# Performance work log

Hardware: AMD Instinct MI355X
Metric: run time of the kernel (lower is better)

## Reference

```python
import jax, jax.numpy as jnp
import numpy as np

N_NODES = 100000
N_EDGES = 3200000
IN_DIM = 768
HIDDEN = 128
CLASS_NUM = 2
N_GRAPHS = 512


def setup_inputs() -> dict:
    key = jax.random.key(0)
    ks = jax.random.split(key, 10)
    x = jax.random.normal(ks[0], (N_NODES, IN_DIM), dtype=jnp.float32)
    edge_index = jax.random.randint(ks[1], (2, N_EDGES), 0, N_NODES, dtype=jnp.int64)
    ptr = jnp.sort(jax.random.randint(ks[2], (N_GRAPHS + 1,), 0, N_NODES, dtype=jnp.int64))
    def glorot(k, shape):
        lim = jnp.sqrt(6.0 / (shape[0] + shape[1]))
        return jax.random.uniform(k, shape, jnp.float32, -lim, lim)
    W1 = glorot(ks[3], (IN_DIM, HIDDEN))
    b1 = jnp.zeros((HIDDEN,), jnp.float32)
    W2 = glorot(ks[4], (HIDDEN, HIDDEN))
    b2 = jnp.zeros((HIDDEN,), jnp.float32)
    Wc = glorot(ks[5], (HIDDEN, CLASS_NUM))
    bc = jnp.zeros((CLASS_NUM,), jnp.float32)
    return {"x": x, "edge_index": edge_index, "ptr": ptr,
            "W1": W1, "b1": b1, "W2": W2, "b2": b2, "Wc": Wc, "bc": bc}


def _gcn_conv(x, W, b, src, dst, norm, n_nodes):
    # PyG GCNConv: linear first, then normalized scatter-add aggregation, then bias
    h = x @ W                                  # [N, out]
    msg = h[src] * norm[:, None]               # gather + scale, [E+N, out]
    out = jax.ops.segment_sum(msg, dst, num_segments=n_nodes)
    return out + b


def reference(x, edge_index, ptr, W1, b1, W2, b2, Wc, bc):
    n = x.shape[0]
    loop = jnp.arange(n, dtype=edge_index.dtype)
    src = jnp.concatenate([edge_index[0], loop])  # add self-loops
    dst = jnp.concatenate([edge_index[1], loop])
    deg = jax.ops.segment_sum(jnp.ones_like(dst, dtype=x.dtype), dst, num_segments=n)
    dinv = jnp.where(deg > 0, jax.lax.rsqrt(deg), 0.0)
    norm = dinv[src] * dinv[dst]               # symmetric normalization
    h = jax.nn.relu(_gcn_conv(x, W1, b1, src, dst, norm, n))
    h = jax.nn.relu(_gcn_conv(h, W2, b2, src, dst, norm, n))
    out = _gcn_conv(h, Wc, bc, src, dst, norm, n)
    return out[ptr[:-1]]                       # first_pool: first node of each graph
```

## Files before the change

kernel.cpp:

```cpp
#include <hip/hip_runtime.h>

typedef short bf16x8 __attribute__((ext_vector_type(8)));
typedef float f32x4 __attribute__((ext_vector_type(4)));
typedef _Float16 f16x4 __attribute__((ext_vector_type(4)));

__device__ __forceinline__ unsigned short f2bf_rn(float x) {
    unsigned int u = __float_as_uint(x);
    unsigned int r = u + 0x7FFF + ((u >> 16) & 1);
    return (unsigned short)(r >> 16);
}
__device__ __forceinline__ float bf2f(unsigned short h) {
    return __uint_as_float(((unsigned int)h) << 16);
}


__global__ __launch_bounds__(256) void bucket_hist(const int* __restrict__ ei,
                                                   int* __restrict__ bcnt, int E, int NB) {
    __shared__ int h[1024];
    for (int i = threadIdx.x; i < NB; i += 256) h[i] = 0;
    __syncthreads();
    for (int e = blockIdx.x * blockDim.x + threadIdx.x; e < E; e += gridDim.x * blockDim.x) {
        atomicAdd(&h[ei[E + e] >> 7], 1);
    }
    __syncthreads();
    for (int i = threadIdx.x; i < NB; i += 256) {
        int v = h[i];
        if (v) atomicAdd(&bcnt[i], v);
    }
}

__global__ __launch_bounds__(1024) void bucket_scan(const int* __restrict__ bcnt,
                                                    int* __restrict__ bbase,
                                                    int* __restrict__ bcur,
                                                    int* __restrict__ offs,
                                                    int NB, int NN, int E) {
    __shared__ int s[1024];
    int t = threadIdx.x;
    int v = (t < NB) ? bcnt[t] : 0;
    s[t] = v;
    __syncthreads();
    for (int off = 1; off < 1024; off <<= 1) {
        int u = (t >= off) ? s[t - off] : 0;
        __syncthreads();
        s[t] += u;
        __syncthreads();
    }
    if (t < NB) {
        int base = s[t] - v;
        bbase[t] = base;
        bcur[t] = base;
    }
    if (t == 0) {
        bbase[NB] = E;
        offs[NN] = E;
    }
}

__global__ __launch_bounds__(256) void bucket_scatter(const int* __restrict__ ei,
                                                      int* __restrict__ bcur,
                                                      unsigned int* __restrict__ epk,
                                                      int E, int NB) {
    __shared__ int hist[1024];
    __shared__ int cur[1024];
    int tid = threadIdx.x;
    int chunk = (E + gridDim.x - 1) / gridDim.x;
    int beg = blockIdx.x * chunk;
    int end = beg + chunk; if (end > E) end = E;
    for (int i = tid; i < NB; i += 256) hist[i] = 0;
    __syncthreads();
    for (int e = beg + tid; e < end; e += 256) {
        atomicAdd(&hist[ei[E + e] >> 7], 1);
    }
    __syncthreads();
    for (int i = tid; i < NB; i += 256) {
        int c = hist[i];
        cur[i] = c ? atomicAdd(&bcur[i], c) : 0;
    }
    __syncthreads();
    for (int e = beg + tid; e < end; e += 256) {
        int s = ei[e];
        int d = ei[E + e];
        int p = atomicAdd(&cur[d >> 7], 1);
        epk[p] = ((unsigned)(d & 127) << 17) | (unsigned)s;
    }
}

__global__ __launch_bounds__(256) void bucket_build(const unsigned int* __restrict__ epk,
                                                    const int* __restrict__ bbase,
                                                    int* __restrict__ offs,
                                                    float* __restrict__ dinv,
                                                    int* __restrict__ srt,
                                                    int NN) {
    __shared__ int lcnt[128];
    __shared__ int sc[128];
    __shared__ int lcur[128];
    int b = blockIdx.x;
    int tid = threadIdx.x;
    int base = bbase[b], endp = bbase[b + 1];
    int ne = endp - base;
    int v0 = b << 7;
    int nv = NN - v0; if (nv > 128) nv = 128;

    if (tid < 128) lcnt[tid] = 0;
    __syncthreads();
    for (int i = tid; i < ne; i += 256) {
        int d = (int)(epk[base + i] >> 17);
        atomicAdd(&lcnt[d], 1);
    }
    __syncthreads();
    if (tid < 128) sc[tid] = lcnt[tid];
    __syncthreads();
    for (int off = 1; off < 128; off <<= 1) {
        int u = (tid < 128 && tid >= off) ? sc[tid - off] : 0;
        __syncthreads();
        if (tid < 128) sc[tid] += u;
        __syncthreads();
    }
    if (tid < nv) {
        int ex = sc[tid] - lcnt[tid];
        offs[v0 + tid] = base + ex;
        lcur[tid] = base + ex;
        dinv[v0 + tid] = rsqrtf((float)(lcnt[tid] + 1));
    }
    __syncthreads();
    for (int i = tid; i < ne; i += 256) {
        unsigned int pk = epk[base + i];
        int d = (int)(pk >> 17);
        int s = (int)(pk & 0x1FFFFu);
        int p = atomicAdd(&lcur[d], 1);
        srt[p] = s << 6;
    }
}

__global__ void wt_prep(const float* __restrict__ W, unsigned short* __restrict__ hi,
                        unsigned short* __restrict__ lo, int K) {
    int idx = blockIdx.x * 256 + threadIdx.x;
    if (idx >= K * 128) return;
    int k = idx >> 7;
    int c = idx & 127;
    float x = W[idx];
    unsigned short h = f2bf_rn(x);
    unsigned short l = f2bf_rn(x - bf2f(h));
    hi[(size_t)c * K + k] = h;
    lo[(size_t)c * K + k] = l;
}

template <int K>
__global__ __launch_bounds__(256) void gemm_mfma(const float* __restrict__ X,
                                                 const unsigned short* __restrict__ Wt_hi,
                                                 const unsigned short* __restrict__ Wt_lo,
                                                 const float* __restrict__ dinv,
                                                 _Float16* __restrict__ G, int n) {
    __shared__ unsigned short As_hi[128][40];
    __shared__ unsigned short As_lo[128][40];
    __shared__ unsigned short Bs_hi[128][40];
    __shared__ unsigned short Bs_lo[128][40];

    const int tid = threadIdx.x;
    const int wave = tid >> 6;
    const int lane = tid & 63;
    const int l15 = lane & 15;
    const int l4 = lane >> 4;
    const int row0 = blockIdx.x * 128;
    const int wr0 = wave * 32;
    const size_t plane = (size_t)n * 32;

    f32x4 acc[2][8];
#pragma unroll
    for (int i = 0; i < 2; ++i)
#pragma unroll
        for (int j = 0; j < 8; ++j) acc[i][j] = (f32x4){0.f, 0.f, 0.f, 0.f};

    const int sr = tid >> 1;
    const int sf = (tid & 1) * 16;

    for (int k0 = 0; k0 < K; k0 += 32) {
        __syncthreads();
        {
            int grow = row0 + sr;
            float4 v[4];
            if (grow < n) {
                const float* src = X + (size_t)grow * K + k0 + sf;
#pragma unroll
                for (int g = 0; g < 4; ++g) v[g] = *(const float4*)(src + g * 4);
            } else {
#pragma unroll
                for (int g = 0; g < 4; ++g) v[g] = make_float4(0.f, 0.f, 0.f, 0.f);
            }
#pragma unroll
            for (int g = 0; g < 4; ++g) {
                ushort4 h, l;
                h.x = f2bf_rn(v[g].x); l.x = f2bf_rn(v[g].x - bf2f(h.x));
                h.y = f2bf_rn(v[g].y); l.y = f2bf_rn(v[g].y - bf2f(h.y));
                h.z = f2bf_rn(v[g].z); l.z = f2bf_rn(v[g].z - bf2f(h.z));
                h.w = f2bf_rn(v[g].w); l.w = f2bf_rn(v[g].w - bf2f(h.w));
                *(ushort4*)&As_hi[sr][sf + g * 4] = h;
                *(ushort4*)&As_lo[sr][sf + g * 4] = l;
            }
        }
        {
#pragma unroll
            for (int rep = 0; rep < 2; ++rep) {
                int id = tid + rep * 256;
                int c = id >> 2;
                int q = (id & 3) * 8;
                *(uint4*)&Bs_hi[c][q] = *(const uint4*)&Wt_hi[(size_t)c * K + k0 + q];
                *(uint4*)&Bs_lo[c][q] = *(const uint4*)&Wt_lo[(size_t)c * K + k0 + q];
            }
        }
        __syncthreads();
        bf16x8 ah[2], al[2];
#pragma unroll
        for (int i = 0; i < 2; ++i) {
            ah[i] = *(const bf16x8*)&As_hi[wr0 + i * 16 + l15][l4 * 8];
            al[i] = *(const bf16x8*)&As_lo[wr0 + i * 16 + l15][l4 * 8];
        }
#pragma unroll
        for (int j = 0; j < 8; ++j) {
            bf16x8 bh = *(const bf16x8*)&Bs_hi[j * 16 + l15][l4 * 8];
            bf16x8 bl = *(const bf16x8*)&Bs_lo[j * 16 + l15][l4 * 8];
#pragma unroll
            for (int i = 0; i < 2; ++i) {
                acc[i][j] = __builtin_amdgcn_mfma_f32_16x16x32_bf16(ah[i], bh, acc[i][j], 0, 0, 0);
                acc[i][j] = __builtin_amdgcn_mfma_f32_16x16x32_bf16(ah[i], bl, acc[i][j], 0, 0, 0);
                acc[i][j] = __builtin_amdgcn_mfma_f32_16x16x32_bf16(al[i], bh, acc[i][j], 0, 0, 0);
            }
        }
    }
#pragma unroll
    for (int i = 0; i < 2; ++i) {
#pragma unroll
        for (int r = 0; r < 4; ++r) {
            int grow = row0 + wr0 + i * 16 + l4 * 4 + r;
            if (grow < n) {
                float dv = dinv[grow];
#pragma unroll
                for (int j = 0; j < 8; ++j) {
                    G[plane * (j >> 1) + (size_t)grow * 32 + (j & 1) * 16 + l15] =
                        (_Float16)(acc[i][j][r] * dv);
                }
            }
        }
    }
}

__global__ __launch_bounds__(256) void aggregate_slice32(const _Float16* __restrict__ G,
                                                         const int* __restrict__ offs,
                                                         const int* __restrict__ srt,
                                                         const float* __restrict__ dinv,
                                                         const float* __restrict__ bias,
                                                         float* __restrict__ H, int n, int do_relu) {
    int bid = blockIdx.x;
    int slice = bid & 3;
    int wave = threadIdx.x >> 6;
    int lane = threadIdx.x & 63;
    int sub = lane >> 5;
    int slot = (lane >> 3) & 3;
    int q = lane & 7;
    int node = (bid >> 2) * 8 + wave * 2 + sub;
    if (node >= n) return;
    const char* __restrict__ Gb = (const char*)G + (size_t)slice * (size_t)n * 64 + q * 8;
    int beg = offs[node], end = offs[node + 1];
    float a0 = 0.f, a1 = 0.f, a2 = 0.f, a3 = 0.f;
    int e = beg + slot;
    for (; e + 12 < end; e += 16) {
        int o0 = srt[e], o1 = srt[e + 4], o2 = srt[e + 8], o3 = srt[e + 12];
        f16x4 v0 = *(const f16x4*)(Gb + o0);
        f16x4 v1 = *(const f16x4*)(Gb + o1);
        f16x4 v2 = *(const f16x4*)(Gb + o2);
        f16x4 v3 = *(const f16x4*)(Gb + o3);
        a0 += (float)v0[0] + (float)v1[0] + (float)v2[0] + (float)v3[0];
        a1 += (float)v0[1] + (float)v1[1] + (float)v2[1] + (float)v3[1];
        a2 += (float)v0[2] + (float)v1[2] + (float)v2[2] + (float)v3[2];
        a3 += (float)v0[3] + (float)v1[3] + (float)v2[3] + (float)v3[3];
    }
    for (; e < end; e += 4) {
        f16x4 v = *(const f16x4*)(Gb + srt[e]);
        a0 += (float)v[0]; a1 += (float)v[1]; a2 += (float)v[2]; a3 += (float)v[3];
    }
    a0 += __shfl_xor(a0, 8);  a1 += __shfl_xor(a1, 8);  a2 += __shfl_xor(a2, 8);  a3 += __shfl_xor(a3, 8);
    a0 += __shfl_xor(a0, 16); a1 += __shfl_xor(a1, 16); a2 += __shfl_xor(a2, 16); a3 += __shfl_xor(a3, 16);
    if (slot == 0) {
        f16x4 sv = *(const f16x4*)(Gb + ((size_t)node << 6));
        a0 += (float)sv[0]; a1 += (float)sv[1]; a2 += (float)sv[2]; a3 += (float)sv[3];
        float dv = dinv[node];
        float4 b = *(const float4*)&bias[slice * 32 + q * 4];
        float4 r;
        r.x = a0 * dv + b.x;
        r.y = a1 * dv + b.y;
        r.z = a2 * dv + b.z;
        r.w = a3 * dv + b.w;
        if (do_relu) {
            r.x = fmaxf(r.x, 0.f); r.y = fmaxf(r.y, 0.f);
            r.z = fmaxf(r.z, 0.f); r.w = fmaxf(r.w, 0.f);
        }
        *(float4*)&H[(size_t)node * 128 + slice * 32 + q * 4] = r;
    }
}

__global__ __launch_bounds__(256) void gemm_c2_kernel(const float* __restrict__ H,
                                                      const float* __restrict__ Wc,
                                                      const float* __restrict__ dinv,
                                                      float* __restrict__ G3, int n) {
    int wid = (blockIdx.x * blockDim.x + threadIdx.x) >> 6;
    int lane = threadIdx.x & 63;
    if (wid >= n) return;
    float2 h = *(const float2*)&H[(size_t)wid * 128 + lane * 2];
    float w00 = Wc[lane * 4 + 0];
    float w01 = Wc[lane * 4 + 1];
    float w10 = Wc[lane * 4 + 2];
    float w11 = Wc[lane * 4 + 3];
    float p0 = h.x * w00 + h.y * w10;
    float p1 = h.x * w01 + h.y * w11;
    for (int off = 32; off > 0; off >>= 1) {
        p0 += __shfl_xor(p0, off);
        p1 += __shfl_xor(p1, off);
    }
    if (lane == 0) {
        float dv = dinv[wid];
        G3[(size_t)wid * 2 + 0] = p0 * dv;
        G3[(size_t)wid * 2 + 1] = p1 * dv;
    }
}

__global__ __launch_bounds__(64) void final_kernel(const float* __restrict__ G3,
                                                   const int* __restrict__ ptr,
                                                   const int* __restrict__ offs,
                                                   const int* __restrict__ srt,
                                                   const float* __restrict__ dinv,
                                                   const float* __restrict__ bc,
                                                   float* __restrict__ out, int ngraphs) {
    int i = blockIdx.x;
    if (i >= ngraphs) return;
    int v = ptr[i];
    int lane = threadIdx.x;
    float p0 = 0.f, p1 = 0.f;
    int beg = offs[v], end = offs[v + 1];
    for (int e = beg + lane; e < end; e += 64) {
        int s = srt[e] >> 6;
        p0 += G3[(size_t)s * 2 + 0];
        p1 += G3[(size_t)s * 2 + 1];
    }
    for (int off = 32; off > 0; off >>= 1) {
        p0 += __shfl_xor(p0, off);
        p1 += __shfl_xor(p1, off);
    }
    if (lane == 0) {
        p0 += G3[(size_t)v * 2 + 0];
        p1 += G3[(size_t)v * 2 + 1];
        float dv = dinv[v];
        out[i * 2 + 0] = p0 * dv + bc[0];
        out[i * 2 + 1] = p1 * dv + bc[1];
    }
}

extern "C" void kernel_launch(void* const* d_in, const int* in_sizes, int n_in,
                              void* d_out, int out_size, void* d_ws, size_t ws_size,
                              hipStream_t stream) {
    const float* x  = (const float*)d_in[0];
    const int* ei   = (const int*)d_in[1];
    const int* ptr  = (const int*)d_in[2];
    const float* W1 = (const float*)d_in[3];
    const float* b1 = (const float*)d_in[4];
    const float* W2 = (const float*)d_in[5];
    const float* b2 = (const float*)d_in[6];
    const float* Wc = (const float*)d_in[7];
    const float* bc = (const float*)d_in[8];
    float* out = (float*)d_out;

    const int IN_DIM = 768, HID = 128;
    const int NN = in_sizes[0] / IN_DIM;
    const int E  = in_sizes[1] / 2;
    const int NG = in_sizes[2] - 1;
    const int NB = (NN + 127) >> 7;

    char* ws = (char*)d_ws;
    size_t off = 0;
    auto alloc = [&](size_t bytes) -> void* {
        void* p = ws + off;
        off += (bytes + 255) & ~(size_t)255;
        return p;
    };
    float* dinv   = (float*)alloc((size_t)NN * 4);
    int*   offs   = (int*)alloc((size_t)(NN + 1) * 4);
    int*   bcnt   = (int*)alloc((size_t)(NB + 1) * 4);
    int*   bbase  = (int*)alloc((size_t)(NB + 1) * 4);
    int*   bcur   = (int*)alloc((size_t)NB * 4);
    int*   srt    = (int*)alloc((size_t)E * 4);
    _Float16* G   = (_Float16*)alloc((size_t)NN * HID * 2);
    float* H      = (float*)alloc((size_t)NN * HID * 4);
    float* G3     = (float*)alloc((size_t)NN * 2 * 4);
    unsigned short* Wt1_hi = (unsigned short*)alloc((size_t)IN_DIM * HID * 2);
    unsigned short* Wt1_lo = (unsigned short*)alloc((size_t)IN_DIM * HID * 2);
    unsigned short* Wt2_hi = (unsigned short*)alloc((size_t)HID * HID * 2);
    unsigned short* Wt2_lo = (unsigned short*)alloc((size_t)HID * HID * 2);

    unsigned int* epk = (unsigned int*)H;

    (void)n_in; (void)out_size; (void)ws_size;

    hipMemsetAsync(bcnt, 0, (size_t)(NB + 1) * 4, stream);
    bucket_hist<<<512, 256, 0, stream>>>(ei, bcnt, E, NB);
    bucket_scan<<<1, 1024, 0, stream>>>(bcnt, bbase, bcur, offs, NB, NN, E);
    bucket_scatter<<<256, 256, 0, stream>>>(ei, bcur, epk, E, NB);
    bucket_build<<<NB, 256, 0, stream>>>(epk, bbase, offs, dinv, srt, NN);

    wt_prep<<<(IN_DIM * HID + 255) / 256, 256, 0, stream>>>(W1, Wt1_hi, Wt1_lo, IN_DIM);
    wt_prep<<<(HID * HID + 255) / 256, 256, 0, stream>>>(W2, Wt2_hi, Wt2_lo, HID);

    int gblocks = (NN + 127) / 128;
    int slice_blocks = ((NN + 7) / 8) * 4;
    int wpn_blocks = (NN * 64 + 255) / 256;

    gemm_mfma<768><<<gblocks, 256, 0, stream>>>(x, Wt1_hi, Wt1_lo, dinv, G, NN);
    aggregate_slice32<<<slice_blocks, 256, 0, stream>>>(G, offs, srt, dinv, b1, H, NN, 1);
    gemm_mfma<128><<<gblocks, 256, 0, stream>>>(H, Wt2_hi, Wt2_lo, dinv, G, NN);
    aggregate_slice32<<<slice_blocks, 256, 0, stream>>>(G, offs, srt, dinv, b2, H, NN, 1);
    gemm_c2_kernel<<<wpn_blocks, 256, 0, stream>>>(H, Wc, dinv, G3, NN);
    final_kernel<<<NG, 64, 0, stream>>>(G3, ptr, offs, srt, dinv, bc, out, NG);
}
```

Measured before the change: 572.6 us.

## Split aggregation into two source-range passes for better gather cache locality

Edges for each destination are partitioned in bucket_build by whether the source lies in the lower or upper half of the nodes, with a per-node midpoint array. Each aggregation is then run as two passes, each gathering from only half of G, so the working set of the random gathers is smaller and more likely to stay in cache. The first pass writes partial sums to H and the second adds them, the self-loop, the scale and the bias. This adds an extra kernel launch and an extra H round trip per layer. The scatter grid size is also doubled.

After: 680.7 us. +18.9%, slower.

```diff
diff --git a/kernel.cpp b/kernel.cpp
--- a/kernel.cpp
+++ b/kernel.cpp
@@ -88,12 +88,15 @@
 __global__ __launch_bounds__(256) void bucket_build(const unsigned int* __restrict__ epk,
                                                     const int* __restrict__ bbase,
                                                     int* __restrict__ offs,
+                                                    int* __restrict__ mids,
                                                     float* __restrict__ dinv,
                                                     int* __restrict__ srt,
-                                                    int NN) {
+                                                    int NN, int NNH) {
     __shared__ int lcnt[128];
+    __shared__ int lcnt0[128];
     __shared__ int sc[128];
-    __shared__ int lcur[128];
+    __shared__ int lcur0[128];
+    __shared__ int lcur1[128];
     int b = blockIdx.x;
     int tid = threadIdx.x;
     int base = bbase[b], endp = bbase[b + 1];
@@ -101,33 +104,39 @@
     int v0 = b << 7;
     int nv = NN - v0; if (nv > 128) nv = 128;
 
-    if (tid < 128) lcnt[tid] = 0;
-    __syncthreads();
-    for (int i = tid; i < ne; i += 256) {
-        int d = (int)(epk[base + i] >> 17);
-        atomicAdd(&lcnt[d], 1);
-    }
-    __syncthreads();
-    if (tid < 128) sc[tid] = lcnt[tid];
-    __syncthreads();
-    for (int off = 1; off < 128; off <<= 1) {
-        int u = (tid < 128 && tid >= off) ? sc[tid - off] : 0;
-        __syncthreads();
-        if (tid < 128) sc[tid] += u;
-        __syncthreads();
-    }
-    if (tid < nv) {
-        int ex = sc[tid] - lcnt[tid];
-        offs[v0 + tid] = base + ex;
-        lcur[tid] = base + ex;
-        dinv[v0 + tid] = rsqrtf((float)(lcnt[tid] + 1));
-    }
+    if (tid < 128) { lcnt[tid] = 0; lcnt0[tid] = 0; }
     __syncthreads();
     for (int i = tid; i < ne; i += 256) {
         unsigned int pk = epk[base + i];
         int d = (int)(pk >> 17);
         int s = (int)(pk & 0x1FFFFu);
-        int p = atomicAdd(&lcur[d], 1);
+        atomicAdd(&lcnt[d], 1);
+        if (s < NNH) atomicAdd(&lcnt0[d], 1);
+    }
+    __syncthreads();
+    if (tid < 128) sc[tid] = lcnt[tid];
+    __syncthreads();
+    for (int off = 1; off < 128; off <<= 1) {
+        int u = (tid < 128 && tid >= off) ? sc[tid - off] : 0;
+        __syncthreads();
+        if (tid < 128) sc[tid] += u;
+        __syncthreads();
+    }
+    if (tid < nv) {
+        int ex = sc[tid] - lcnt[tid];
+        int p0 = base + ex;
+        offs[v0 + tid] = p0;
+        mids[v0 + tid] = p0 + lcnt0[tid];
+        lcur0[tid] = p0;
+        lcur1[tid] = p0 + lcnt0[tid];
+        dinv[v0 + tid] = rsqrtf((float)(lcnt[tid] + 1));
+    }
+    __syncthreads();
+    for (int i = tid; i < ne; i += 256) {
+        unsigned int pk = epk[base + i];
+        int d = (int)(pk >> 17);
+        int s = (int)(pk & 0x1FFFFu);
+        int p = (s < NNH) ? atomicAdd(&lcur0[d], 1) : atomicAdd(&lcur1[d], 1);
         srt[p] = s << 6;
     }
 }
@@ -245,11 +254,13 @@
 }
 
 __global__ __launch_bounds__(256) void aggregate_slice32(const _Float16* __restrict__ G,
-                                                         const int* __restrict__ offs,
+                                                         const int* __restrict__ lo,
+                                                         const int* __restrict__ hi,
                                                          const int* __restrict__ srt,
                                                          const float* __restrict__ dinv,
                                                          const float* __restrict__ bias,
-                                                         float* __restrict__ H, int n, int do_relu) {
+                                                         float* __restrict__ H, int n,
+                                                         int do_relu, int pass2) {
     int bid = blockIdx.x;
     int slice = bid & 3;
     int wave = threadIdx.x >> 6;
@@ -260,7 +271,7 @@
     int node = (bid >> 2) * 8 + wave * 2 + sub;
     if (node >= n) return;
     const char* __restrict__ Gb = (const char*)G + (size_t)slice * (size_t)n * 64 + q * 8;
-    int beg = offs[node], end = offs[node + 1];
+    int beg = lo[node], end = hi[node];
     float a0 = 0.f, a1 = 0.f, a2 = 0.f, a3 = 0.f;
     int e = beg + slot;
     for (; e + 12 < end; e += 16) {
@@ -281,20 +292,29 @@
     a0 += __shfl_xor(a0, 8);  a1 += __shfl_xor(a1, 8);  a2 += __shfl_xor(a2, 8);  a3 += __shfl_xor(a3, 8);
     a0 += __shfl_xor(a0, 16); a1 += __shfl_xor(a1, 16); a2 += __shfl_xor(a2, 16); a3 += __shfl_xor(a3, 16);
     if (slot == 0) {
-        f16x4 sv = *(const f16x4*)(Gb + ((size_t)node << 6));
-        a0 += (float)sv[0]; a1 += (float)sv[1]; a2 += (float)sv[2]; a3 += (float)sv[3];
-        float dv = dinv[node];
-        float4 b = *(const float4*)&bias[slice * 32 + q * 4];
-        float4 r;
-        r.x = a0 * dv + b.x;
-        r.y = a1 * dv + b.y;
-        r.z = a2 * dv + b.z;
-        r.w = a3 * dv + b.w;
-        if (do_relu) {
-            r.x = fmaxf(r.x, 0.f); r.y = fmaxf(r.y, 0.f);
-            r.z = fmaxf(r.z, 0.f); r.w = fmaxf(r.w, 0.f);
-        }
-        *(float4*)&H[(size_t)node * 128 + slice * 32 + q * 4] = r;
+        float* hp = &H[(size_t)node * 128 + slice * 32 + q * 4];
+        if (!pass2) {
+            *(float4*)hp = make_float4(a0, a1, a2, a3);
+        } else {
+            f16x4 sv = *(const f16x4*)(Gb + ((size_t)node << 6));
+            float4 p = *(const float4*)hp;
+            a0 += p.x + (float)sv[0];
+            a1 += p.y + (float)sv[1];
+            a2 += p.z + (float)sv[2];
+            a3 += p.w + (float)sv[3];
+            float dv = dinv[node];
+            float4 b = *(const float4*)&bias[slice * 32 + q * 4];
+            float4 r;
+            r.x = a0 * dv + b.x;
+            r.y = a1 * dv + b.y;
+            r.z = a2 * dv + b.z;
+            r.w = a3 * dv + b.w;
+            if (do_relu) {
+                r.x = fmaxf(r.x, 0.f); r.y = fmaxf(r.y, 0.f);
+                r.z = fmaxf(r.z, 0.f); r.w = fmaxf(r.w, 0.f);
+            }
+            *(float4*)hp = r;
+        }
     }
 }
 
@@ -373,6 +393,7 @@
     const int E  = in_sizes[1] / 2;
     const int NG = in_sizes[2] - 1;
     const int NB = (NN + 127) >> 7;
+    const int NNH = NN >> 1;
 
     char* ws = (char*)d_ws;
     size_t off = 0;
@@ -383,6 +404,7 @@
     };
     float* dinv   = (float*)alloc((size_t)NN * 4);
     int*   offs   = (int*)alloc((size_t)(NN + 1) * 4);
+    int*   mids   = (int*)alloc((size_t)NN * 4);
     int*   bcnt   = (int*)alloc((size_t)(NB + 1) * 4);
     int*   bbase  = (int*)alloc((size_t)(NB + 1) * 4);
     int*   bcur   = (int*)alloc((size_t)NB * 4);
@@ -402,8 +424,8 @@
     hipMemsetAsync(bcnt, 0, (size_t)(NB + 1) * 4, stream);
     bucket_hist<<<512, 256, 0, stream>>>(ei, bcnt, E, NB);
     bucket_scan<<<1, 1024, 0, stream>>>(bcnt, bbase, bcur, offs, NB, NN, E);
-    bucket_scatter<<<256, 256, 0, stream>>>(ei, bcur, epk, E, NB);
-    bucket_build<<<NB, 256, 0, stream>>>(epk, bbase, offs, dinv, srt, NN);
+    bucket_scatter<<<512, 256, 0, stream>>>(ei, bcur, epk, E, NB);
+    bucket_build<<<NB, 256, 0, stream>>>(epk, bbase, offs, mids, dinv, srt, NN, NNH);
 
     wt_prep<<<(IN_DIM * HID + 255) / 256, 256, 0, stream>>>(W1, Wt1_hi, Wt1_lo, IN_DIM);
     wt_prep<<<(HID * HID + 255) / 256, 256, 0, stream>>>(W2, Wt2_hi, Wt2_lo, HID);
@@ -413,9 +435,11 @@
     int wpn_blocks = (NN * 64 + 255) / 256;
 
     gemm_mfma<768><<<gblocks, 256, 0, stream>>>(x, Wt1_hi, Wt1_lo, dinv, G, NN);
-    aggregate_slice32<<<slice_blocks, 256, 0, stream>>>(G, offs, srt, dinv, b1, H, NN, 1);
+    aggregate_slice32<<<slice_blocks, 256, 0, stream>>>(G, offs, mids, srt, dinv, b1, H, NN, 1, 0);
+    aggregate_slice32<<<slice_blocks, 256, 0, stream>>>(G, mids, offs + 1, srt, dinv, b1, H, NN, 1, 1);
     gemm_mfma<128><<<gblocks, 256, 0, stream>>>(H, Wt2_hi, Wt2_lo, dinv, G, NN);
-    aggregate_slice32<<<slice_blocks, 256, 0, stream>>>(G, offs, srt, dinv, b2, H, NN, 1);
+    aggregate_slice32<<<slice_blocks, 256, 0, stream>>>(G, offs, mids, srt, dinv, b2, H, NN, 1, 0);
+    aggregate_slice32<<<slice_blocks, 256, 0, stream>>>(G, mids, offs + 1, srt, dinv, b2, H, NN, 1, 1);
     gemm_c2_kernel<<<wpn_blocks, 256, 0, stream>>>(H, Wc, dinv, G3, NN);
     final_kernel<<<NG, 64, 0, stream>>>(G3, ptr, offs, srt, dinv, bc, out, NG);
 }
```
